# Performance work log

Measured on AMD Instinct MI355X. Metric: run time of the kernel, lower is better.

## Reference

```python
import jax, jax.numpy as jnp
import numpy as np

K = 8  # kernel_size
COUT = 512


def setup_inputs() -> dict:
    key = jax.random.key(0)
    k1, k2, k3 = jax.random.split(key, 3)
    B, CIN, L = 8, 512, 2048
    x = jax.random.normal(k1, (B, CIN, L), dtype=jnp.float32)
    # nn.Linear(CIN, COUT*K) weight, scaled like kaiming-uniform-ish init
    W = jax.random.normal(k2, (COUT * K, CIN), dtype=jnp.float32) * (1.0 / np.sqrt(CIN))
    b = jax.random.normal(k3, (COUT,), dtype=jnp.float32)
    return {"x": x, "W": W, "b": b}


def reference(x, W, b):
    # x: (B, Cin, L); W: (Cout*K, Cin) with row layout j = k*Cout + co; b: (Cout,)
    B, Cin, L = x.shape
    # pointwise linear expand: (B, Cout*K, L)
    z = jnp.einsum('bcl,oc->bol', x, W)
    z = z.reshape(B, K, COUT, L)  # k-major channel layout
    # causal overlap-add fold: y[b,co,t] = sum_k z[b,k,co,t-k]
    y = z[:, 0]
    for k in range(1, K):  # small fixed kernel-size loop
        y = y.at[:, :, k:].add(z[:, k, :, : L - k])
    return y + b[None, :, None]
```

## Files before the change

### kernel.cpp

```cpp
#include <hip/hip_runtime.h>
#include <hip/hip_bf16.h>
#include <cstdint>
#include <cstddef>

#define CIN   512
#define COUT  512
#define LLEN  2048
#define BATCH 8
#define KTAP  8
#define LPAD  (LLEN + 8)

typedef __bf16 bf16x8_t __attribute__((ext_vector_type(8)));
typedef float  f32x4_t  __attribute__((ext_vector_type(4)));
typedef unsigned short u16x8_t __attribute__((ext_vector_type(8)));

__device__ __forceinline__ unsigned short f2bf(float f) {
  __bf16 h = (__bf16)f;
  return __builtin_bit_cast(unsigned short, h);
}

__device__ __forceinline__ void gl2lds16(unsigned short* lds, const unsigned short* g) {
  __builtin_amdgcn_global_load_lds(
      (const __attribute__((address_space(1))) unsigned int*)g,
      (__attribute__((address_space(3))) unsigned int*)lds,
      16, 0, 0);
}

__global__ __launch_bounds__(256) void prepass_kernel(
    const float* __restrict__ x, unsigned short* __restrict__ xtp,
    const float4* __restrict__ W, u16x8_t* __restrict__ Wb) {
  const int bid = blockIdx.x;
  const int t   = threadIdx.x;

  if (bid >= 2048) {
    int idx = (bid - 2048) * 256 + t;
    float4 a = W[idx * 2], b = W[idx * 2 + 1];
    u16x8_t o;
    o[0] = f2bf(a.x); o[1] = f2bf(a.y); o[2] = f2bf(a.z); o[3] = f2bf(a.w);
    o[4] = f2bf(b.x); o[5] = f2bf(b.y); o[6] = f2bf(b.z); o[7] = f2bf(b.w);
    Wb[idx] = o;
    return;
  }

  __shared__ float tile[64][65];
  const int b  = bid >> 8;
  const int c0 = ((bid >> 5) & 7) * 64;
  const int l0 = (bid & 31) * 64;

  if ((bid & 31) == 0 && t < 64) {
    unsigned short* hp = xtp + ((size_t)b * LPAD + (t >> 3)) * CIN + c0 + (t & 7) * 8;
    *(u16x8_t*)hp = (u16x8_t){0, 0, 0, 0, 0, 0, 0, 0};
  }

  {
    const int cr = t >> 2;
    const int lv = (t & 3) * 16;
    const float* src = x + ((size_t)b * CIN + c0 + cr) * LLEN + l0 + lv;
#pragma unroll
    for (int i = 0; i < 4; ++i) {
      float4 v = *(const float4*)(src + 4 * i);
      tile[cr][lv + 4 * i + 0] = v.x;
      tile[cr][lv + 4 * i + 1] = v.y;
      tile[cr][lv + 4 * i + 2] = v.z;
      tile[cr][lv + 4 * i + 3] = v.w;
    }
  }
  __syncthreads();
  {
    const int l    = t >> 2;
    const int cseg = (t & 3) * 16;
    unsigned short ov[16];
#pragma unroll
    for (int u = 0; u < 16; ++u) ov[u] = f2bf(tile[cseg + u][l]);
    unsigned short* dst = xtp + ((size_t)b * LPAD + 8 + l0 + l) * CIN + c0 + cseg;
    *(u16x8_t*)dst       = *(const u16x8_t*)&ov[0];
    *(u16x8_t*)(dst + 8) = *(const u16x8_t*)&ov[8];
  }
}


__global__ __launch_bounds__(128) void conv_gemm_kernel(
    const unsigned short* __restrict__ Wb,
    const unsigned short* __restrict__ xtp,
    const float* __restrict__ bias,
    float* __restrict__ y)
{
  __shared__ __align__(16) unsigned short As[2][128 * 64];
  __shared__ __align__(16) unsigned short Bs[2][136 * 64];

  const int t    = threadIdx.x;
  const int lane = t & 63;
  const int wv   = t >> 6;
  const int l0   = blockIdx.x * 128;
  const int o0   = blockIdx.y * 128;
  const int b    = blockIdx.z;

  const int quad = lane >> 4;
  const int lrow = lane & 15;

  f32x4_t acc[8][4];
#pragma unroll
  for (int i = 0; i < 8; ++i)
#pragma unroll
    for (int j = 0; j < 4; ++j)
      acc[i][j] = (f32x4_t){0.f, 0.f, 0.f, 0.f};

  const int srow    = t >> 3;
  const int schunk  = (t & 7) ^ (srow & 7);
  const int lds_off = t * 8;

  const unsigned short* xb = xtp + (size_t)b * LPAD * CIN;

  auto stage_A = [&](int kk, int buf) {
    const unsigned short* asrc =
        Wb + (size_t)((kk & 7) * COUT + o0 + srow) * CIN + (kk >> 3) * 64 + schunk * 8;
#pragma unroll
    for (int rd = 0; rd < 8; ++rd)
      gl2lds16(&As[buf][0] + lds_off + rd * 1024, asrc + (size_t)rd * 16 * CIN);
  };
  auto stage_B = [&](int ct, int buf) {
    const int c0 = ct * 64;
    const unsigned short* src = xb + (size_t)(l0 + srow) * CIN + c0 + schunk * 8;
#pragma unroll
    for (int rd = 0; rd < 8; ++rd)
      gl2lds16(&Bs[buf][0] + lds_off + rd * 1024, src + (size_t)rd * 16 * CIN);
    if (t < 64) {
      const int r2  = 128 + (t >> 3);
      const int ch2 = (t & 7) ^ (r2 & 7);
      gl2lds16(&Bs[buf][0] + 128 * 64 + t * 8,
               xb + (size_t)(l0 + r2) * CIN + c0 + ch2 * 8);
    }
  };

  stage_B(0, 0);
  stage_A(0, 0);
  __syncthreads();

#pragma unroll 1
  for (int kk = 0; kk < 64; ++kk) {
    const int k  = kk & 7;
    const int ct = kk >> 3;
    if (kk + 1 < 64) stage_A(kk + 1, (kk + 1) & 1);
    if (k == 7 && ct + 1 < 8) stage_B(ct + 1, (ct + 1) & 1);

    const unsigned short* Ac = &As[kk & 1][0];
    const unsigned short* Bc = &Bs[ct & 1][0];
    const int bshift = 8 - k;

#pragma unroll
    for (int h = 0; h < 2; ++h) {
      bf16x8_t af[8], bfr[4];
#pragma unroll
      for (int i = 0; i < 8; ++i) {
        int row  = i * 16 + lrow;
        int slot = (h * 4 + quad) ^ (row & 7);
        af[i] = *(const bf16x8_t*)(Ac + row * 64 + slot * 8);
      }
#pragma unroll
      for (int j = 0; j < 4; ++j) {
        int row  = bshift + wv * 64 + j * 16 + lrow;
        int slot = (h * 4 + quad) ^ (row & 7);
        bfr[j] = *(const bf16x8_t*)(Bc + row * 64 + slot * 8);
      }
#pragma unroll
      for (int i = 0; i < 8; ++i)
#pragma unroll
        for (int j = 0; j < 4; ++j)
          acc[i][j] = __builtin_amdgcn_mfma_f32_16x16x32_bf16(af[i], bfr[j], acc[i][j], 0, 0, 0);
    }
    __syncthreads();
  }

#pragma unroll
  for (int i = 0; i < 8; ++i) {
    const int o_base = o0 + i * 16 + quad * 4;
    const float4 bv = *(const float4*)(bias + o_base);
    const float bvr[4] = {bv.x, bv.y, bv.z, bv.w};
#pragma unroll
    for (int j = 0; j < 4; ++j) {
      const int l = l0 + wv * 64 + j * 16 + lrow;
#pragma unroll
      for (int r = 0; r < 4; ++r) {
        y[((size_t)b * COUT + o_base + r) * LLEN + l] = acc[i][j][r] + bvr[r];
      }
    }
  }
}


extern "C" void kernel_launch(void* const* d_in, const int* in_sizes, int n_in,
                              void* d_out, int out_size, void* d_ws, size_t ws_size,
                              hipStream_t stream) {
  const float* x    = (const float*)d_in[0];
  const float* W    = (const float*)d_in[1];
  const float* bias = (const float*)d_in[2];
  float* y          = (float*)d_out;

  unsigned short* xtp = (unsigned short*)d_ws;
  unsigned short* Wb  = (unsigned short*)((char*)d_ws +
                        (size_t)BATCH * LPAD * CIN * sizeof(unsigned short));

  prepass_kernel<<<2048 + 1024, 256, 0, stream>>>(
      x, xtp, (const float4*)W, (u16x8_t*)Wb);
  conv_gemm_kernel<<<dim3(LLEN / 128, COUT / 128, BATCH), 128, 0, stream>>>(
      Wb, xtp, bias, y);
}
```

Baseline: 163.8 us.

## Halve GEMM output-channel tile, single-buffer B tile, and recoalesce prepass transpose

The conv GEMM tile shrinks from 128 to 64 output channels per block, which halves the accumulator registers and the A-tile LDS. The grid doubles from 512 to 1024 blocks, giving more blocks in flight on the 256-CU part. The B tile drops from double to single buffering, so its reload now runs between two barriers without overlap, once every 8 iterations. The prepass transpose changes its thread mapping so that global loads are contiguous across threads and each thread stores 8 bf16 values per row. The risks are more total A/B traffic per FLOP, lower MFMA density per block, and the exposed B load stall.

```diff
diff --git a/kernel.cpp b/kernel.cpp
--- a/kernel.cpp
+++ b/kernel.cpp
@@ -53,28 +53,31 @@
   }
 
   {
-    const int cr = t >> 2;
-    const int lv = (t & 3) * 16;
-    const float* src = x + ((size_t)b * CIN + c0 + cr) * LLEN + l0 + lv;
-#pragma unroll
-    for (int i = 0; i < 4; ++i) {
-      float4 v = *(const float4*)(src + 4 * i);
-      tile[cr][lv + 4 * i + 0] = v.x;
-      tile[cr][lv + 4 * i + 1] = v.y;
-      tile[cr][lv + 4 * i + 2] = v.z;
-      tile[cr][lv + 4 * i + 3] = v.w;
+    const int cr = t >> 4;
+    const int lv = (t & 15) * 4;
+#pragma unroll
+    for (int rd = 0; rd < 4; ++rd) {
+      const int c = cr + rd * 16;
+      float4 v = *(const float4*)(x + ((size_t)b * CIN + c0 + c) * LLEN + l0 + lv);
+      tile[c][lv + 0] = v.x;
+      tile[c][lv + 1] = v.y;
+      tile[c][lv + 2] = v.z;
+      tile[c][lv + 3] = v.w;
     }
   }
   __syncthreads();
   {
-    const int l    = t >> 2;
-    const int cseg = (t & 3) * 16;
-    unsigned short ov[16];
-#pragma unroll
-    for (int u = 0; u < 16; ++u) ov[u] = f2bf(tile[cseg + u][l]);
-    unsigned short* dst = xtp + ((size_t)b * LPAD + 8 + l0 + l) * CIN + c0 + cseg;
-    *(u16x8_t*)dst       = *(const u16x8_t*)&ov[0];
-    *(u16x8_t*)(dst + 8) = *(const u16x8_t*)&ov[8];
+    const int lr   = t >> 3;
+    const int cseg = (t & 7) * 8;
+#pragma unroll
+    for (int rd = 0; rd < 2; ++rd) {
+      const int l = lr + rd * 32;
+      unsigned short ov[8];
+#pragma unroll
+      for (int u = 0; u < 8; ++u) ov[u] = f2bf(tile[cseg + u][l]);
+      unsigned short* dst = xtp + ((size_t)b * LPAD + 8 + l0 + l) * CIN + c0 + cseg;
+      *(u16x8_t*)dst = *(const u16x8_t*)&ov[0];
+    }
   }
 }
 
@@ -85,22 +88,22 @@
     const float* __restrict__ bias,
     float* __restrict__ y)
 {
-  __shared__ __align__(16) unsigned short As[2][128 * 64];
-  __shared__ __align__(16) unsigned short Bs[2][136 * 64];
+  __shared__ __align__(16) unsigned short As[2][64 * 64];
+  __shared__ __align__(16) unsigned short Bs[136 * 64];
 
   const int t    = threadIdx.x;
   const int lane = t & 63;
   const int wv   = t >> 6;
   const int l0   = blockIdx.x * 128;
-  const int o0   = blockIdx.y * 128;
+  const int o0   = blockIdx.y * 64;
   const int b    = blockIdx.z;
 
   const int quad = lane >> 4;
   const int lrow = lane & 15;
 
-  f32x4_t acc[8][4];
-#pragma unroll
-  for (int i = 0; i < 8; ++i)
+  f32x4_t acc[4][4];
+#pragma unroll
+  for (int i = 0; i < 4; ++i)
 #pragma unroll
     for (int j = 0; j < 4; ++j)
       acc[i][j] = (f32x4_t){0.f, 0.f, 0.f, 0.f};
@@ -115,24 +118,24 @@
     const unsigned short* asrc =
         Wb + (size_t)((kk & 7) * COUT + o0 + srow) * CIN + (kk >> 3) * 64 + schunk * 8;
 #pragma unroll
-    for (int rd = 0; rd < 8; ++rd)
+    for (int rd = 0; rd < 4; ++rd)
       gl2lds16(&As[buf][0] + lds_off + rd * 1024, asrc + (size_t)rd * 16 * CIN);
   };
-  auto stage_B = [&](int ct, int buf) {
+  auto stage_B = [&](int ct) {
     const int c0 = ct * 64;
     const unsigned short* src = xb + (size_t)(l0 + srow) * CIN + c0 + schunk * 8;
 #pragma unroll
     for (int rd = 0; rd < 8; ++rd)
-      gl2lds16(&Bs[buf][0] + lds_off + rd * 1024, src + (size_t)rd * 16 * CIN);
+      gl2lds16(&Bs[0] + lds_off + rd * 1024, src + (size_t)rd * 16 * CIN);
     if (t < 64) {
       const int r2  = 128 + (t >> 3);
       const int ch2 = (t & 7) ^ (r2 & 7);
-      gl2lds16(&Bs[buf][0] + 128 * 64 + t * 8,
+      gl2lds16(&Bs[0] + 128 * 64 + t * 8,
                xb + (size_t)(l0 + r2) * CIN + c0 + ch2 * 8);
     }
   };
 
-  stage_B(0, 0);
+  stage_B(0);
   stage_A(0, 0);
   __syncthreads();
 
@@ -141,17 +144,15 @@
     const int k  = kk & 7;
     const int ct = kk >> 3;
     if (kk + 1 < 64) stage_A(kk + 1, (kk + 1) & 1);
-    if (k == 7 && ct + 1 < 8) stage_B(ct + 1, (ct + 1) & 1);
 
     const unsigned short* Ac = &As[kk & 1][0];
-    const unsigned short* Bc = &Bs[ct & 1][0];
     const int bshift = 8 - k;
 
 #pragma unroll
     for (int h = 0; h < 2; ++h) {
-      bf16x8_t af[8], bfr[4];
-#pragma unroll
-      for (int i = 0; i < 8; ++i) {
+      bf16x8_t af[4], bfr[4];
+#pragma unroll
+      for (int i = 0; i < 4; ++i) {
         int row  = i * 16 + lrow;
         int slot = (h * 4 + quad) ^ (row & 7);
         af[i] = *(const bf16x8_t*)(Ac + row * 64 + slot * 8);
@@ -160,19 +161,26 @@
       for (int j = 0; j < 4; ++j) {
         int row  = bshift + wv * 64 + j * 16 + lrow;
         int slot = (h * 4 + quad) ^ (row & 7);
-        bfr[j] = *(const bf16x8_t*)(Bc + row * 64 + slot * 8);
+        bfr[j] = *(const bf16x8_t*)(Bs + row * 64 + slot * 8);
       }
 #pragma unroll
-      for (int i = 0; i < 8; ++i)
+      for (int i = 0; i < 4; ++i)
 #pragma unroll
         for (int j = 0; j < 4; ++j)
           acc[i][j] = __builtin_amdgcn_mfma_f32_16x16x32_bf16(af[i], bfr[j], acc[i][j], 0, 0, 0);
     }
-    __syncthreads();
-  }
-
-#pragma unroll
-  for (int i = 0; i < 8; ++i) {
+
+    if (k == 7 && ct + 1 < 8) {
+      __syncthreads();
+      stage_B(ct + 1);
+      __syncthreads();
+    } else {
+      __syncthreads();
+    }
+  }
+
+#pragma unroll
+  for (int i = 0; i < 4; ++i) {
     const int o_base = o0 + i * 16 + quad * 4;
     const float4 bv = *(const float4*)(bias + o_base);
     const float bvr[4] = {bv.x, bv.y, bv.z, bv.w};
@@ -202,6 +210,6 @@
 
   prepass_kernel<<<2048 + 1024, 256, 0, stream>>>(
       x, xtp, (const float4*)W, (u16x8_t*)Wb);
-  conv_gemm_kernel<<<dim3(LLEN / 128, COUT / 128, BATCH), 128, 0, stream>>>(
+  conv_gemm_kernel<<<dim3(LLEN / 128, COUT / 64, BATCH), 128, 0, stream>>>(
       Wb, xtp, bias, y);
 }
```

Measured after the change: 150.4 us. -8.2%, faster.
